# Kernel optimization log

Hardware: AMD Instinct MI355X
Metric: run time of the kernel (lower is better)

Reference implementation:

```python
import jax, jax.numpy as jnp
import numpy as np

F_DIM = 256; L = 4; B = 1; H = 160; W = 160; FH = 1024; N = B * H * W

def _ln(x, w, b):
    mu = jnp.mean(x, -1, keepdims=True)
    var = jnp.mean(jnp.square(x - mu), -1, keepdims=True)
    return (x - mu) * jax.lax.rsqrt(var + 1e-5) * w + b

def _conv(x, w, b, groups=1, pad=0):
    y = jax.lax.conv_general_dilated(x, w, (1, 1), [(pad, pad), (pad, pad)],
                                     dimension_numbers=('NCHW', 'OIHW', 'NCHW'),
                                     feature_group_count=groups)
    return y + b[None, :, None, None]

def _wsilu(x):
    return jax.nn.sigmoid(4.0 * x) * x

def setup_inputs() -> dict:
    key = jax.random.key(0)
    ks = iter(jax.random.split(key, 40))
    nk = lambda: next(ks)
    s = 1.0 / np.sqrt(F_DIM).astype(np.float32)
    inp = {}
    inp['x'] = jax.random.normal(nk(), (B, 1, H, W), jnp.float32)
    inp['cin_w1'] = jax.random.normal(nk(), (F_DIM, 1, 1, 1), jnp.float32)
    inp['cin_b1'] = jnp.zeros((F_DIM,), jnp.float32)
    inp['cin_w2'] = jax.random.normal(nk(), (F_DIM, 1, 7, 7), jnp.float32) * 0.15
    inp['cin_b2'] = jnp.zeros((F_DIM,), jnp.float32)
    inp['ln0_w'] = jnp.ones((F_DIM,), jnp.float32); inp['ln0_b'] = jnp.zeros((F_DIM,), jnp.float32)
    inp['ln1_w'] = jnp.ones((L, F_DIM), jnp.float32); inp['ln1_b'] = jnp.zeros((L, F_DIM), jnp.float32)
    inp['ln2_w'] = jnp.ones((L, F_DIM), jnp.float32); inp['ln2_b'] = jnp.zeros((L, F_DIM), jnp.float32)
    for n in ['att_tmk', 'att_tmv', 'att_tmr', 'ffn_tmk', 'ffn_tmr']:
        inp[n] = jax.random.uniform(nk(), (L, F_DIM), jnp.float32)
    inp['att_tf'] = jax.random.normal(nk(), (L, F_DIM), jnp.float32) * 0.5
    # time_decay is stored as -exp(raw) by the module's loader
    inp['att_td'] = -jnp.exp(jax.random.normal(nk(), (L, F_DIM), jnp.float32) * 0.5)
    for n in ['att_kw', 'att_vw', 'att_rw', 'att_ow', 'ffn_rw']:
        inp[n] = jax.random.normal(nk(), (L, F_DIM, F_DIM), jnp.float32) * s
    inp['ffn_kw'] = jax.random.normal(nk(), (L, FH, F_DIM), jnp.float32) * s
    inp['ffn_vw'] = jax.random.normal(nk(), (L, F_DIM, FH), jnp.float32) * (1.0 / np.sqrt(FH).astype(np.float32))
    inp['spa_dw_w'] = jax.random.normal(nk(), (L, F_DIM, 1, 7, 7), jnp.float32) * 0.15
    inp['spa_dw_b'] = jnp.zeros((L, F_DIM), jnp.float32)
    inp['spa_pw_w'] = jax.random.normal(nk(), (L, F_DIM, F_DIM, 1, 1), jnp.float32) * s
    inp['spa_pw_b'] = jnp.zeros((L, F_DIM), jnp.float32)
    st = jnp.zeros((5 * L, N, F_DIM), jnp.float32)
    st = st.at[4::5].add(-1e30)  # pp slots start at -1e30 as in torch init
    inp['state0'] = st
    return inp

def reference(x, cin_w1, cin_b1, cin_w2, cin_b2, ln0_w, ln0_b, ln1_w, ln1_b,
              ln2_w, ln2_b, att_tmk, att_tmv, att_tmr, att_tf, att_td,
              att_kw, att_vw, att_rw, att_ow, ffn_tmk, ffn_tmr, ffn_kw,
              ffn_vw, ffn_rw, spa_dw_w, spa_dw_b, spa_pw_w, spa_pw_b, state0):
    # conv stem: 1x1 -> depthwise 7x7 -> WSiLU
    d = _conv(x, cin_w1, cin_b1)
    d = _wsilu(_conv(d, cin_w2, cin_b2, groups=F_DIM, pad=3))
    d = d.transpose(0, 2, 3, 1).reshape(N, F_DIM)  # 'b f h w -> (b h w) f'
    for i in range(L):
        if i == 0:
            d = _ln(d, ln0_w, ln0_b)
        # --- SA: single-step RWKV WKV ---
        xs = _ln(d, ln1_w[i], ln1_b[i])
        sp = state0[5 * i + 1]
        aa = state0[5 * i + 2]; bb = state0[5 * i + 3]; pp = state0[5 * i + 4]
        xk = xs * att_tmk[i] + sp * (1 - att_tmk[i])
        xv = xs * att_tmv[i] + sp * (1 - att_tmv[i])
        xr = xs * att_tmr[i] + sp * (1 - att_tmr[i])
        r = jax.nn.sigmoid(xr @ att_rw[i].T)
        k = xk @ att_kw[i].T
        v = xv @ att_vw[i].T
        ww = att_tf[i] + k
        p = jnp.maximum(pp, ww)
        e1 = jnp.exp(pp - p); e2 = jnp.exp(ww - p)
        wkv = (e1 * aa + e2 * v) / (e1 * bb + e2)
        d = d + (r * wkv) @ att_ow[i].T
        # --- FF: squared-relu channel mix ---
        xs = _ln(d, ln2_w[i], ln2_b[i])
        sp = state0[5 * i + 0]
        xk = xs * ffn_tmk[i] + sp * (1 - ffn_tmk[i])
        xr = xs * ffn_tmr[i] + sp * (1 - ffn_tmr[i])
        rr = jax.nn.sigmoid(xr @ ffn_rw[i].T)
        kk = jnp.square(jax.nn.relu(xk @ ffn_kw[i].T))
        d = d + rr * (kk @ ffn_vw[i].T)
        # --- spatial residual block ---
        img = d.reshape(B, H, W, F_DIM).transpose(0, 3, 1, 2)
        img = img + _conv(_conv(img, spa_dw_w[i], spa_dw_b[i], groups=F_DIM, pad=3),
                          spa_pw_w[i], spa_pw_b[i])
        d = img.transpose(0, 2, 3, 1).reshape(N, F_DIM)
    return d.reshape(B, H, W, F_DIM).transpose(0, 3, 1, 2)
```

## Files before the change

kernel.cpp:

```cpp
#include <hip/hip_runtime.h>
#include <hip/hip_bf16.h>
#include <cstdint>
#include <cstddef>

#define F_DIMC 256
#define FHC    1024
#define IMGH   160
#define IMGW   160
#define NTOK   25600
#define NLAY   4

using bf16 = __hip_bfloat16;
typedef __attribute__((ext_vector_type(8))) short bf16x8;
typedef __attribute__((ext_vector_type(4))) float f32x4;

#define MFMA16(a, b, c) __builtin_amdgcn_mfma_f32_16x16x32_bf16((a), (b), (c), 0, 0, 0)

struct Cvt6 { const float* s[6]; bf16* d[6]; };
__global__ void cvt6_k(Cvt6 a, int n) {
    int z = blockIdx.y;
    int i = blockIdx.x * 256 + threadIdx.x;
    if (i < n) a.d[z][i] = __float2bfloat16(a.s[z][i]);
}
struct Cvt2 { const float* s[2]; bf16* d[2]; };
__global__ void cvt2_k(Cvt2 a, int n) {
    int z = blockIdx.y;
    int i = blockIdx.x * 256 + threadIdx.x;
    if (i < n) a.d[z][i] = __float2bfloat16(a.s[z][i]);
}

__global__ void dw_transpose_k(const float* __restrict__ src, float* __restrict__ dst, int n) {
    int i = blockIdx.x * 256 + threadIdx.x;
    if (i < n) {
        int f = i & (F_DIMC - 1);
        int lt = i >> 8;
        int t = lt % 49;
        int l = lt / 49;
        dst[i] = src[((size_t)l * F_DIMC + f) * 49 + t];
    }
}

__global__ __launch_bounds__(256)
void stem2_k(const float* __restrict__ x, const float* __restrict__ w1,
             const float* __restrict__ b1, const float* __restrict__ w2,
             const float* __restrict__ b2, float* __restrict__ d)
{
    __shared__ float wts[49][64];
    __shared__ float w1s[64], b1s[64], b2s[64];
    __shared__ float2 xp[7][22];
    const int tid = threadIdx.x;
    const int f0 = blockIdx.y * 64;
    const int y = blockIdx.x / 10;
    const int x0 = (blockIdx.x % 10) * 16;

    for (int idx = tid; idx < 49 * 64; idx += 256) {
        int t = idx >> 6, fl = idx & 63;
        wts[t][fl] = w2[(f0 + fl) * 49 + t];
    }
    if (tid < 64) {
        w1s[tid] = w1[f0 + tid];
        b1s[tid] = b1[f0 + tid];
        b2s[tid] = b2[f0 + tid];
    }
    for (int p = tid; p < 7 * 22; p += 256) {
        int py = p / 22, px = p % 22;
        int gy = y + py - 3, gx = x0 + px - 3;
        bool ok = (unsigned)gy < IMGH && (unsigned)gx < IMGW;
        xp[py][px] = ok ? make_float2(x[gy * IMGW + gx], 1.f) : make_float2(0.f, 0.f);
    }
    __syncthreads();

    const int fl = tid & 63;
    const int xbase = (tid >> 6) * 4;
    float acc[4] = {0.f, 0.f, 0.f, 0.f}, accw[4] = {0.f, 0.f, 0.f, 0.f};
    #pragma unroll
    for (int ky = 0; ky < 7; ++ky) {
        float2 row[10];
        #pragma unroll
        for (int q = 0; q < 10; ++q) row[q] = xp[ky][xbase + q];
        #pragma unroll
        for (int kx = 0; kx < 7; ++kx) {
            float w = wts[ky * 7 + kx][fl];
            #pragma unroll
            for (int j = 0; j < 4; ++j) {
                acc[j]  = fmaf(row[j + kx].x, w, acc[j]);
                accw[j] = fmaf(row[j + kx].y, w, accw[j]);
            }
        }
    }
    const float w1f = w1s[fl], b1f = b1s[fl], b2f = b2s[fl];
    #pragma unroll
    for (int j = 0; j < 4; ++j) {
        float u = fmaf(w1f, acc[j], fmaf(b1f, accw[j], b2f));
        int pix = y * IMGW + x0 + xbase + j;
        d[(size_t)pix * F_DIMC + f0 + fl] = u / (1.f + __expf(-4.f * u));
    }
}

__device__ __forceinline__ void wave_ln(float* x, const float* __restrict__ w,
                                        const float* __restrict__ b, int lane)
{
    float s = x[0] + x[1] + x[2] + x[3];
    #pragma unroll
    for (int m = 1; m < 64; m <<= 1) s += __shfl_xor(s, m, 64);
    float mu = s * 0.00390625f;
    float t0 = x[0] - mu, t1 = x[1] - mu, t2 = x[2] - mu, t3 = x[3] - mu;
    float v = t0 * t0 + t1 * t1 + t2 * t2 + t3 * t3;
    #pragma unroll
    for (int m = 1; m < 64; m <<= 1) v += __shfl_xor(v, m, 64);
    float inv = rsqrtf(v * 0.00390625f + 1e-5f);
    f32x4 wv = *(const f32x4*)(w + lane * 4);
    f32x4 bv = *(const f32x4*)(b + lane * 4);
    x[0] = t0 * inv * wv[0] + bv[0];
    x[1] = t1 * inv * wv[1] + bv[1];
    x[2] = t2 * inv * wv[2] + bv[2];
    x[3] = t3 * inv * wv[3] + bv[3];
}

union Pack4 { bf16 h[4]; uint2 u; };

template<bool LN0>
__global__ __launch_bounds__(256)
void lnmix_sa_k(float* __restrict__ d, const float* __restrict__ sp,
                const float* __restrict__ ln0w, const float* __restrict__ ln0b,
                const float* __restrict__ lnw, const float* __restrict__ lnb,
                const float* __restrict__ tmk, const float* __restrict__ tmv,
                const float* __restrict__ tmr,
                bf16* __restrict__ xk, bf16* __restrict__ xv, bf16* __restrict__ xr)
{
    const int lane = threadIdx.x & 63;
    const int n = blockIdx.x * 4 + (threadIdx.x >> 6);
    const int base = n * F_DIMC + lane * 4;
    f32x4 dv = *(const f32x4*)(d + base);
    float xo[4] = {dv[0], dv[1], dv[2], dv[3]};
    if (LN0) {
        wave_ln(xo, ln0w, ln0b, lane);
        f32x4 o = {xo[0], xo[1], xo[2], xo[3]};
        *(f32x4*)(d + base) = o;
    }
    float xs[4] = {xo[0], xo[1], xo[2], xo[3]};
    wave_ln(xs, lnw, lnb, lane);
    f32x4 spv = *(const f32x4*)(sp + base);
    f32x4 k4 = *(const f32x4*)(tmk + lane * 4);
    f32x4 v4 = *(const f32x4*)(tmv + lane * 4);
    f32x4 r4 = *(const f32x4*)(tmr + lane * 4);
    Pack4 pk, pv, pr;
    #pragma unroll
    for (int j = 0; j < 4; ++j) {
        pk.h[j] = __float2bfloat16(xs[j] * k4[j] + spv[j] * (1.f - k4[j]));
        pv.h[j] = __float2bfloat16(xs[j] * v4[j] + spv[j] * (1.f - v4[j]));
        pr.h[j] = __float2bfloat16(xs[j] * r4[j] + spv[j] * (1.f - r4[j]));
    }
    *(uint2*)(xk + base) = pk.u;
    *(uint2*)(xv + base) = pv.u;
    *(uint2*)(xr + base) = pr.u;
}

__global__ __launch_bounds__(256)
void lnmix_ff_k(const float* __restrict__ d, const float* __restrict__ sp,
                const float* __restrict__ lnw, const float* __restrict__ lnb,
                const float* __restrict__ tmk, const float* __restrict__ tmr,
                bf16* __restrict__ xk, bf16* __restrict__ xr)
{
    const int lane = threadIdx.x & 63;
    const int n = blockIdx.x * 4 + (threadIdx.x >> 6);
    const int base = n * F_DIMC + lane * 4;
    f32x4 dv = *(const f32x4*)(d + base);
    float xs[4] = {dv[0], dv[1], dv[2], dv[3]};
    wave_ln(xs, lnw, lnb, lane);
    f32x4 spv = *(const f32x4*)(sp + base);
    f32x4 k4 = *(const f32x4*)(tmk + lane * 4);
    f32x4 r4 = *(const f32x4*)(tmr + lane * 4);
    Pack4 pk, pr;
    #pragma unroll
    for (int j = 0; j < 4; ++j) {
        pk.h[j] = __float2bfloat16(xs[j] * k4[j] + spv[j] * (1.f - k4[j]));
        pr.h[j] = __float2bfloat16(xs[j] * r4[j] + spv[j] * (1.f - r4[j]));
    }
    *(uint2*)(xk + base) = pk.u;
    *(uint2*)(xr + base) = pr.u;
}


__device__ __forceinline__ void stage_swz32(const bf16* __restrict__ g,
                                            bf16* lds, int tid)
{
    #pragma unroll
    for (int s = 0; s < 8; ++s) {
        int chunk = s * 256 + tid;
        int row = chunk >> 5, c16 = chunk & 31;
        int gc = c16 ^ (row & 15);
        __builtin_amdgcn_global_load_lds(
            (const __attribute__((address_space(1))) void*)(g + (size_t)row * 256 + gc * 8),
            (__attribute__((address_space(3))) void*)(lds + chunk * 8), 16, 0, 0);
    }
}

__device__ __forceinline__ void stage_swz16(const bf16* __restrict__ g, int lda,
                                            bf16* lds, int tid)
{
    #pragma unroll
    for (int s = 0; s < 8; ++s) {
        int chunk = s * 256 + tid;
        int row = chunk >> 4, c16 = chunk & 15;
        int gc = c16 ^ (row & 15);
        __builtin_amdgcn_global_load_lds(
            (const __attribute__((address_space(1))) void*)(g + (size_t)row * lda + gc * 8),
            (__attribute__((address_space(3))) void*)(lds + chunk * 8), 16, 0, 0);
    }
}

template<int RB>
__device__ __forceinline__ bf16x8 frag_ld(const bf16* lds, int row, int cb)
{
    return *(const bf16x8*)((const char*)lds + row * RB + (cb ^ ((row & 15) << 4)));
}

__device__ __forceinline__ void pass64(const bf16* __restrict__ Ag, const bf16* __restrict__ Bg,
                                       bf16* As, bf16* Bs, int tid, int wr, int wc,
                                       int lr, int hi, f32x4 (&acc)[2][2])
{
    stage_swz32(Ag, As, tid);
    stage_swz32(Bg, Bs, tid);
    __syncthreads();
    #pragma unroll
    for (int ks = 0; ks < 8; ++ks) {
        int cb = ks * 64 + hi * 16;
        bf16x8 a0 = frag_ld<512>(As, wr * 32 + lr, cb);
        bf16x8 a1 = frag_ld<512>(As, wr * 32 + 16 + lr, cb);
        bf16x8 b0 = frag_ld<512>(Bs, wc * 32 + lr, cb);
        bf16x8 b1 = frag_ld<512>(Bs, wc * 32 + 16 + lr, cb);
        acc[0][0] = MFMA16(a0, b0, acc[0][0]);
        acc[0][1] = MFMA16(a0, b1, acc[0][1]);
        acc[1][0] = MFMA16(a1, b0, acc[1][0]);
        acc[1][1] = MFMA16(a1, b1, acc[1][1]);
    }
    __syncthreads();
}

__global__ __launch_bounds__(256, 2)
void sawkv_k(const bf16* __restrict__ xk, const bf16* __restrict__ xv,
             const bf16* __restrict__ xr,
             const bf16* __restrict__ kw, const bf16* __restrict__ vw,
             const bf16* __restrict__ rw,
             const float* __restrict__ aa, const float* __restrict__ bb,
             const float* __restrict__ pp, const float* __restrict__ tf,
             bf16* __restrict__ ab)
{
    __shared__ __align__(16) bf16 As[64 * 256];
    __shared__ __align__(16) bf16 Bs[64 * 256];
    const int tid = threadIdx.x, lane = tid & 63, wave = tid >> 6;
    const int wr = wave >> 1, wc = wave & 1;
    const int lr = lane & 15, hi = lane >> 4;
    const int m0 = blockIdx.x * 64, n0 = blockIdx.y * 64;

    f32x4 ak[2][2], av[2][2], ar[2][2];
    #pragma unroll
    for (int m = 0; m < 2; ++m)
        #pragma unroll
        for (int n = 0; n < 2; ++n) {
            ak[m][n] = (f32x4){0.f, 0.f, 0.f, 0.f};
            av[m][n] = (f32x4){0.f, 0.f, 0.f, 0.f};
            ar[m][n] = (f32x4){0.f, 0.f, 0.f, 0.f};
        }

    pass64(xk + (size_t)m0 * 256, kw + (size_t)n0 * 256, As, Bs, tid, wr, wc, lr, hi, ak);
    pass64(xv + (size_t)m0 * 256, vw + (size_t)n0 * 256, As, Bs, tid, wr, wc, lr, hi, av);
    pass64(xr + (size_t)m0 * 256, rw + (size_t)n0 * 256, As, Bs, tid, wr, wc, lr, hi, ar);

    const int lr0 = hi * 4;
    #pragma unroll
    for (int mf = 0; mf < 2; ++mf)
        #pragma unroll
        for (int nf = 0; nf < 2; ++nf) {
            int col = n0 + wc * 32 + nf * 16 + lr;
            float tfc = tf[col];
            #pragma unroll
            for (int j = 0; j < 4; ++j) {
                int row = m0 + wr * 32 + mf * 16 + lr0 + j;
                size_t idx = (size_t)row * F_DIMC + col;
                float kk = ak[mf][nf][j], vv = av[mf][nf][j], rr = ar[mf][nf][j];
                float P = pp[idx];
                float ww = tfc + kk;
                float p = fmaxf(P, ww);
                float e1 = __expf(P - p), e2 = __expf(ww - p);
                float wkv = (e1 * aa[idx] + e2 * vv) / (e1 * bb[idx] + e2);
                ab[idx] = __float2bfloat16(wkv / (1.f + __expf(-rr)));
            }
        }
}

template<int EPI>
__global__ __launch_bounds__(256, 2)
void gemm128_k(const bf16* __restrict__ A, const bf16* __restrict__ Bw,
               int lda, int ldb, int K, int Nout,
               float* __restrict__ Cf, bf16* __restrict__ Cb,
               const float* __restrict__ bias)
{
    __shared__ __align__(16) bf16 As[128 * 128];
    __shared__ __align__(16) bf16 Bs[128 * 128];
    const int tid = threadIdx.x, lane = tid & 63, wave = tid >> 6;
    const int wr = wave >> 1, wc = wave & 1;
    const int lr = lane & 15, hi = lane >> 4;
    const int m0 = blockIdx.x * 128, n0 = blockIdx.y * 128;

    f32x4 acc[4][4];
    #pragma unroll
    for (int m = 0; m < 4; ++m)
        #pragma unroll
        for (int n = 0; n < 4; ++n) acc[m][n] = (f32x4){0.f, 0.f, 0.f, 0.f};

    for (int kt = 0; kt < K; kt += 128) {
        stage_swz16(A + (size_t)m0 * lda + kt, lda, As, tid);
        stage_swz16(Bw + (size_t)n0 * ldb + kt, ldb, Bs, tid);
        __syncthreads();
        #pragma unroll
        for (int ks = 0; ks < 4; ++ks) {
            int cb = ks * 64 + hi * 16;
            bf16x8 a[4], b[4];
            #pragma unroll
            for (int mf = 0; mf < 4; ++mf) a[mf] = frag_ld<256>(As, wr * 64 + mf * 16 + lr, cb);
            #pragma unroll
            for (int nf = 0; nf < 4; ++nf) b[nf] = frag_ld<256>(Bs, wc * 64 + nf * 16 + lr, cb);
            #pragma unroll
            for (int mf = 0; mf < 4; ++mf)
                #pragma unroll
                for (int nf = 0; nf < 4; ++nf)
                    acc[mf][nf] = MFMA16(a[mf], b[nf], acc[mf][nf]);
        }
        __syncthreads();
    }

    const int lr0 = hi * 4;
    #pragma unroll
    for (int mf = 0; mf < 4; ++mf)
        #pragma unroll
        for (int nf = 0; nf < 4; ++nf) {
            int col = n0 + wc * 64 + nf * 16 + lr;
            #pragma unroll
            for (int j = 0; j < 4; ++j) {
                int row = m0 + wr * 64 + mf * 16 + lr0 + j;
                size_t cidx = (size_t)row * Nout + col;
                float v = acc[mf][nf][j];
                if constexpr (EPI == 2) { float t = fmaxf(v, 0.f); Cb[cidx] = __float2bfloat16(t * t); }
                else if constexpr (EPI == 3) Cf[cidx] += v;
                else if constexpr (EPI == 5) Cf[cidx] += v + bias[col];
            }
        }
}

__global__ __launch_bounds__(256, 2)
void fvwrr_k(const bf16* __restrict__ kkb, const bf16* __restrict__ fvw,
             const bf16* __restrict__ xr, const bf16* __restrict__ rw,
             float* __restrict__ d)
{
    __shared__ __align__(16) bf16 As[128 * 128];
    __shared__ __align__(16) bf16 Bs[128 * 128];
    const int tid = threadIdx.x, lane = tid & 63, wave = tid >> 6;
    const int wr = wave >> 1, wc = wave & 1;
    const int lr = lane & 15, hi = lane >> 4;
    const int m0 = blockIdx.x * 128, n0 = blockIdx.y * 128;

    f32x4 arr[4][4], am[4][4];
    #pragma unroll
    for (int m = 0; m < 4; ++m)
        #pragma unroll
        for (int n = 0; n < 4; ++n) {
            arr[m][n] = (f32x4){0.f, 0.f, 0.f, 0.f};
            am[m][n]  = (f32x4){0.f, 0.f, 0.f, 0.f};
        }

    for (int kt = 0; kt < 256; kt += 128) {
        stage_swz16(xr + (size_t)m0 * 256 + kt, 256, As, tid);
        stage_swz16(rw + (size_t)n0 * 256 + kt, 256, Bs, tid);
        __syncthreads();
        #pragma unroll
        for (int ks = 0; ks < 4; ++ks) {
            int cb = ks * 64 + hi * 16;
            bf16x8 a[4], b[4];
            #pragma unroll
            for (int mf = 0; mf < 4; ++mf) a[mf] = frag_ld<256>(As, wr * 64 + mf * 16 + lr, cb);
            #pragma unroll
            for (int nf = 0; nf < 4; ++nf) b[nf] = frag_ld<256>(Bs, wc * 64 + nf * 16 + lr, cb);
            #pragma unroll
            for (int mf = 0; mf < 4; ++mf)
                #pragma unroll
                for (int nf = 0; nf < 4; ++nf)
                    arr[mf][nf] = MFMA16(a[mf], b[nf], arr[mf][nf]);
        }
        __syncthreads();
    }
    for (int kt = 0; kt < 1024; kt += 128) {
        stage_swz16(kkb + (size_t)m0 * 1024 + kt, 1024, As, tid);
        stage_swz16(fvw + (size_t)n0 * 1024 + kt, 1024, Bs, tid);
        __syncthreads();
        #pragma unroll
        for (int ks = 0; ks < 4; ++ks) {
            int cb = ks * 64 + hi * 16;
            bf16x8 a[4], b[4];
            #pragma unroll
            for (int mf = 0; mf < 4; ++mf) a[mf] = frag_ld<256>(As, wr * 64 + mf * 16 + lr, cb);
            #pragma unroll
            for (int nf = 0; nf < 4; ++nf) b[nf] = frag_ld<256>(Bs, wc * 64 + nf * 16 + lr, cb);
            #pragma unroll
            for (int mf = 0; mf < 4; ++mf)
                #pragma unroll
                for (int nf = 0; nf < 4; ++nf)
                    am[mf][nf] = MFMA16(a[mf], b[nf], am[mf][nf]);
        }
        __syncthreads();
    }

    const int lr0 = hi * 4;
    #pragma unroll
    for (int mf = 0; mf < 4; ++mf)
        #pragma unroll
        for (int nf = 0; nf < 4; ++nf) {
            int col = n0 + wc * 64 + nf * 16 + lr;
            #pragma unroll
            for (int j = 0; j < 4; ++j) {
                int row = m0 + wr * 64 + mf * 16 + lr0 + j;
                size_t cidx = (size_t)row * F_DIMC + col;
                float rr = 1.f / (1.f + __expf(-arr[mf][nf][j]));
                d[cidx] += rr * am[mf][nf][j];
            }
        }
}

__global__ __launch_bounds__(256)
void dwconv2_k(const float* __restrict__ d, const float* __restrict__ wT,
               const float* __restrict__ bias, bf16* __restrict__ out)
{
    __shared__ float patch[196][64];
    __shared__ float wt[49][64];
    const int lane = threadIdx.x;
    const int ty = threadIdx.y;
    const int f0 = blockIdx.z * 64;
    const int w0 = blockIdx.x * 8, h0 = blockIdx.y * 8;

    for (int t = ty; t < 49; t += 4) wt[t][lane] = wT[t * F_DIMC + f0 + lane];
    for (int p = ty; p < 196; p += 4) {
        int py = p / 14, px = p % 14;
        int gy = h0 + py - 3, gx = w0 + px - 3;
        float v = 0.f;
        if ((unsigned)gy < IMGH && (unsigned)gx < IMGW)
            v = d[(size_t)(gy * IMGW + gx) * F_DIMC + f0 + lane];
        patch[p][lane] = v;
    }
    __syncthreads();

    const float b = bias[f0 + lane];
    #pragma unroll
    for (int rr = 0; rr < 2; ++rr) {
        int ry = ty * 2 + rr;
        float acc8[8];
        #pragma unroll
        for (int px = 0; px < 8; ++px) acc8[px] = b;
        #pragma unroll
        for (int ky = 0; ky < 7; ++ky) {
            float rowv[14];
            #pragma unroll
            for (int c = 0; c < 14; ++c) rowv[c] = patch[(ry + ky) * 14 + c][lane];
            #pragma unroll
            for (int kx = 0; kx < 7; ++kx) {
                float w = wt[ky * 7 + kx][lane];
                #pragma unroll
                for (int px = 0; px < 8; ++px)
                    acc8[px] = fmaf(rowv[px + kx], w, acc8[px]);
            }
        }
        #pragma unroll
        for (int px = 0; px < 8; ++px)
            out[(size_t)((h0 + ry) * IMGW + (w0 + px)) * F_DIMC + f0 + lane] = __float2bfloat16(acc8[px]);
    }
}

__global__ __launch_bounds__(256)
void transpose_out_k(const float* __restrict__ d, float* __restrict__ out)
{
    __shared__ float tile[32][33];
    const int n0 = blockIdx.x * 32, f0 = blockIdx.y * 32;
    const int tx = threadIdx.x, ty = threadIdx.y;
    for (int r = ty; r < 32; r += 8) tile[r][tx] = d[(size_t)(n0 + r) * F_DIMC + f0 + tx];
    __syncthreads();
    for (int r = ty; r < 32; r += 8) out[(size_t)(f0 + r) * NTOK + n0 + tx] = tile[tx][r];
}

extern "C" void kernel_launch(void* const* d_in, const int* in_sizes, int n_in,
                              void* d_out, int out_size, void* d_ws, size_t ws_size,
                              hipStream_t stream)
{
    if (n_in < 30) return;
    const float* x        = (const float*)d_in[0];
    const float* cin_w1   = (const float*)d_in[1];
    const float* cin_b1   = (const float*)d_in[2];
    const float* cin_w2   = (const float*)d_in[3];
    const float* cin_b2   = (const float*)d_in[4];
    const float* ln0_w    = (const float*)d_in[5];
    const float* ln0_b    = (const float*)d_in[6];
    const float* ln1_w    = (const float*)d_in[7];
    const float* ln1_b    = (const float*)d_in[8];
    const float* ln2_w    = (const float*)d_in[9];
    const float* ln2_b    = (const float*)d_in[10];
    const float* att_tmk  = (const float*)d_in[11];
    const float* att_tmv  = (const float*)d_in[12];
    const float* att_tmr  = (const float*)d_in[13];
    const float* ffn_tmk  = (const float*)d_in[14];
    const float* ffn_tmr  = (const float*)d_in[15];
    const float* att_tf   = (const float*)d_in[16];
    const float* att_kw   = (const float*)d_in[18];
    const float* att_vw   = (const float*)d_in[19];
    const float* att_rw   = (const float*)d_in[20];
    const float* att_ow   = (const float*)d_in[21];
    const float* ffn_rw   = (const float*)d_in[22];
    const float* ffn_kw   = (const float*)d_in[23];
    const float* ffn_vw   = (const float*)d_in[24];
    const float* spa_dw_w = (const float*)d_in[25];
    const float* spa_dw_b = (const float*)d_in[26];
    const float* spa_pw_w = (const float*)d_in[27];
    const float* spa_pw_b = (const float*)d_in[28];
    const float* state0   = (const float*)d_in[29];
    float* out = (float*)d_out;

    const size_t NF = (size_t)NTOK * F_DIMC;
    char* wsp = (char*)d_ws;
    size_t off = 0;
    auto alloc = [&](size_t bytes) -> void* {
        void* p = wsp + off;
        off += (bytes + 255) & ~(size_t)255;
        return p;
    };
    float* d_buf = (float*)alloc(NF * 4);
    bf16*  xk    = (bf16*)alloc(NF * 2);
    bf16*  xv    = (bf16*)alloc(NF * 2);
    bf16*  xr    = (bf16*)alloc(NF * 2);
    bf16*  ab    = (bf16*)alloc(NF * 2);
    bf16*  kkb   = (bf16*)alloc((size_t)NTOK * FHC * 2);
    const size_t WSQ = (size_t)NLAY * F_DIMC * F_DIMC;
    bf16* kwb  = (bf16*)alloc(WSQ * 2);
    bf16* vwb  = (bf16*)alloc(WSQ * 2);
    bf16* rwb  = (bf16*)alloc(WSQ * 2);
    bf16* owb  = (bf16*)alloc(WSQ * 2);
    bf16* frwb = (bf16*)alloc(WSQ * 2);
    bf16* fkwb = (bf16*)alloc((size_t)NLAY * FHC * F_DIMC * 2);
    bf16* fvwb = (bf16*)alloc((size_t)NLAY * F_DIMC * FHC * 2);
    bf16* pwb  = (bf16*)alloc(WSQ * 2);
    float* dwT = (float*)alloc((size_t)NLAY * 49 * F_DIMC * 4);
    if (off > ws_size) return;

    {
        Cvt6 c6;
        c6.s[0] = att_kw;  c6.d[0] = kwb;
        c6.s[1] = att_vw;  c6.d[1] = vwb;
        c6.s[2] = att_rw;  c6.d[2] = rwb;
        c6.s[3] = att_ow;  c6.d[3] = owb;
        c6.s[4] = ffn_rw;  c6.d[4] = frwb;
        c6.s[5] = spa_pw_w; c6.d[5] = pwb;
        cvt6_k<<<dim3(((int)WSQ + 255) / 256, 6), dim3(256), 0, stream>>>(c6, (int)WSQ);
        Cvt2 c2;
        c2.s[0] = ffn_kw; c2.d[0] = fkwb;
        c2.s[1] = ffn_vw; c2.d[1] = fvwb;
        int n2 = NLAY * FHC * F_DIMC;
        cvt2_k<<<dim3((n2 + 255) / 256, 2), dim3(256), 0, stream>>>(c2, n2);
        int n = NLAY * 49 * F_DIMC;
        dw_transpose_k<<<dim3((n + 255) / 256), dim3(256), 0, stream>>>(spa_dw_w, dwT, n);
    }

    stem2_k<<<dim3(IMGH * 10, 4), dim3(256), 0, stream>>>(x, cin_w1, cin_b1, cin_w2, cin_b2, d_buf);

    for (int i = 0; i < NLAY; ++i) {
        const float* sp_ff = state0 + (size_t)(5 * i + 0) * NF;
        const float* sp_at = state0 + (size_t)(5 * i + 1) * NF;
        const float* aa    = state0 + (size_t)(5 * i + 2) * NF;
        const float* bb    = state0 + (size_t)(5 * i + 3) * NF;
        const float* pp    = state0 + (size_t)(5 * i + 4) * NF;
        const float* l1w = ln1_w + i * F_DIMC, *l1b = ln1_b + i * F_DIMC;
        const float* l2w = ln2_w + i * F_DIMC, *l2b = ln2_b + i * F_DIMC;
        const float* tmk = att_tmk + i * F_DIMC, *tmv = att_tmv + i * F_DIMC, *tmr = att_tmr + i * F_DIMC;
        const float* ftmk = ffn_tmk + i * F_DIMC, *ftmr = ffn_tmr + i * F_DIMC;
        const float* tf = att_tf + i * F_DIMC;
        const bf16* kw_i  = kwb  + (size_t)i * F_DIMC * F_DIMC;
        const bf16* vw_i  = vwb  + (size_t)i * F_DIMC * F_DIMC;
        const bf16* rw_i  = rwb  + (size_t)i * F_DIMC * F_DIMC;
        const bf16* ow_i  = owb  + (size_t)i * F_DIMC * F_DIMC;
        const bf16* frw_i = frwb + (size_t)i * F_DIMC * F_DIMC;
        const bf16* fkw_i = fkwb + (size_t)i * FHC * F_DIMC;
        const bf16* fvw_i = fvwb + (size_t)i * F_DIMC * FHC;
        const bf16* pw_i  = pwb  + (size_t)i * F_DIMC * F_DIMC;
        const float* dwT_i = dwT + (size_t)i * 49 * F_DIMC;
        const float* dwb_i = spa_dw_b + i * F_DIMC;
        const float* pwbias_i = spa_pw_b + i * F_DIMC;

        if (i == 0)
            lnmix_sa_k<true><<<dim3(NTOK / 4), dim3(256), 0, stream>>>(
                d_buf, sp_at, ln0_w, ln0_b, l1w, l1b, tmk, tmv, tmr, xk, xv, xr);
        else
            lnmix_sa_k<false><<<dim3(NTOK / 4), dim3(256), 0, stream>>>(
                d_buf, sp_at, ln0_w, ln0_b, l1w, l1b, tmk, tmv, tmr, xk, xv, xr);

        sawkv_k<<<dim3(NTOK / 64, 4), dim3(256), 0, stream>>>(
            xk, xv, xr, kw_i, vw_i, rw_i, aa, bb, pp, tf, ab);

        gemm128_k<3><<<dim3(NTOK / 128, 2), dim3(256), 0, stream>>>(
            ab, ow_i, F_DIMC, F_DIMC, F_DIMC, F_DIMC, d_buf, nullptr, nullptr);

        lnmix_ff_k<<<dim3(NTOK / 4), dim3(256), 0, stream>>>(d_buf, sp_ff, l2w, l2b, ftmk, ftmr, xk, xr);

        gemm128_k<2><<<dim3(NTOK / 128, 8), dim3(256), 0, stream>>>(
            xk, fkw_i, F_DIMC, F_DIMC, F_DIMC, FHC, nullptr, kkb, nullptr);

        fvwrr_k<<<dim3(NTOK / 128, 2), dim3(256), 0, stream>>>(kkb, fvw_i, xr, frw_i, d_buf);

        dwconv2_k<<<dim3(IMGW / 8, IMGH / 8, 4), dim3(64, 4), 0, stream>>>(d_buf, dwT_i, dwb_i, ab);

        gemm128_k<5><<<dim3(NTOK / 128, 2), dim3(256), 0, stream>>>(
            ab, pw_i, F_DIMC, F_DIMC, F_DIMC, F_DIMC, d_buf, nullptr, pwbias_i);
    }

    transpose_out_k<<<dim3(NTOK / 32, F_DIMC / 32), dim3(32, 8), 0, stream>>>(d_buf, out);
}
```

Baseline: 1.952 ms.

## Store residual in fp16 and split KV/R projection from WKV elementwise

Converts the residual stream buffer from fp32 to fp16 throughout all kernels that read or update it, halving its memory traffic. Replaces the fused 64x64 three-pass K/V/R GEMM plus WKV epilogue with a batched 128x128 GEMM writing fp16 K, V and sigmoid(R), followed by a separate elementwise WKV kernel. Makes the GEMM K dimension a compile-time template parameter with unrolled loops. The split adds extra intermediate round trips, and accumulating residual updates in fp16 risks precision loss.

After: 1.931 ms. About the same (-1.1%).

```diff
diff --git a/kernel.cpp b/kernel.cpp
--- a/kernel.cpp
+++ b/kernel.cpp
@@ -11,10 +11,14 @@
 #define NLAY   4
 
 using bf16 = __hip_bfloat16;
+using f16  = _Float16;
 typedef __attribute__((ext_vector_type(8))) short bf16x8;
 typedef __attribute__((ext_vector_type(4))) float f32x4;
 
 #define MFMA16(a, b, c) __builtin_amdgcn_mfma_f32_16x16x32_bf16((a), (b), (c), 0, 0, 0)
+
+union H4 { f16 h[4]; uint2 u; };
+union Pack4 { bf16 h[4]; uint2 u; };
 
 struct Cvt6 { const float* s[6]; bf16* d[6]; };
 __global__ void cvt6_k(Cvt6 a, int n) {
@@ -43,7 +47,7 @@
 __global__ __launch_bounds__(256)
 void stem2_k(const float* __restrict__ x, const float* __restrict__ w1,
              const float* __restrict__ b1, const float* __restrict__ w2,
-             const float* __restrict__ b2, float* __restrict__ d)
+             const float* __restrict__ b2, f16* __restrict__ d)
 {
     __shared__ float wts[49][64];
     __shared__ float w1s[64], b1s[64], b2s[64];
@@ -93,7 +97,7 @@
     for (int j = 0; j < 4; ++j) {
         float u = fmaf(w1f, acc[j], fmaf(b1f, accw[j], b2f));
         int pix = y * IMGW + x0 + xbase + j;
-        d[(size_t)pix * F_DIMC + f0 + fl] = u / (1.f + __expf(-4.f * u));
+        d[(size_t)pix * F_DIMC + f0 + fl] = (f16)(u / (1.f + __expf(-4.f * u)));
     }
 }
 
@@ -117,11 +121,9 @@
     x[3] = t3 * inv * wv[3] + bv[3];
 }
 
-union Pack4 { bf16 h[4]; uint2 u; };
-
 template<bool LN0>
 __global__ __launch_bounds__(256)
-void lnmix_sa_k(float* __restrict__ d, const float* __restrict__ sp,
+void lnmix_sa_k(f16* __restrict__ d, const float* __restrict__ sp,
                 const float* __restrict__ ln0w, const float* __restrict__ ln0b,
                 const float* __restrict__ lnw, const float* __restrict__ lnb,
                 const float* __restrict__ tmk, const float* __restrict__ tmv,
@@ -131,12 +133,14 @@
     const int lane = threadIdx.x & 63;
     const int n = blockIdx.x * 4 + (threadIdx.x >> 6);
     const int base = n * F_DIMC + lane * 4;
-    f32x4 dv = *(const f32x4*)(d + base);
-    float xo[4] = {dv[0], dv[1], dv[2], dv[3]};
+    H4 hv; hv.u = *(const uint2*)(d + base);
+    float xo[4] = {(float)hv.h[0], (float)hv.h[1], (float)hv.h[2], (float)hv.h[3]};
     if (LN0) {
         wave_ln(xo, ln0w, ln0b, lane);
-        f32x4 o = {xo[0], xo[1], xo[2], xo[3]};
-        *(f32x4*)(d + base) = o;
+        H4 o;
+        #pragma unroll
+        for (int j = 0; j < 4; ++j) o.h[j] = (f16)xo[j];
+        *(uint2*)(d + base) = o.u;
     }
     float xs[4] = {xo[0], xo[1], xo[2], xo[3]};
     wave_ln(xs, lnw, lnb, lane);
@@ -157,7 +161,7 @@
 }
 
 __global__ __launch_bounds__(256)
-void lnmix_ff_k(const float* __restrict__ d, const float* __restrict__ sp,
+void lnmix_ff_k(const f16* __restrict__ d, const float* __restrict__ sp,
                 const float* __restrict__ lnw, const float* __restrict__ lnb,
                 const float* __restrict__ tmk, const float* __restrict__ tmr,
                 bf16* __restrict__ xk, bf16* __restrict__ xr)
@@ -165,8 +169,8 @@
     const int lane = threadIdx.x & 63;
     const int n = blockIdx.x * 4 + (threadIdx.x >> 6);
     const int base = n * F_DIMC + lane * 4;
-    f32x4 dv = *(const f32x4*)(d + base);
-    float xs[4] = {dv[0], dv[1], dv[2], dv[3]};
+    H4 hv; hv.u = *(const uint2*)(d + base);
+    float xs[4] = {(float)hv.h[0], (float)hv.h[1], (float)hv.h[2], (float)hv.h[3]};
     wave_ln(xs, lnw, lnb, lane);
     f32x4 spv = *(const f32x4*)(sp + base);
     f32x4 k4 = *(const f32x4*)(tmk + lane * 4);
@@ -181,19 +185,32 @@
     *(uint2*)(xr + base) = pr.u;
 }
 
-
-__device__ __forceinline__ void stage_swz32(const bf16* __restrict__ g,
-                                            bf16* lds, int tid)
-{
-    #pragma unroll
-    for (int s = 0; s < 8; ++s) {
-        int chunk = s * 256 + tid;
-        int row = chunk >> 5, c16 = chunk & 31;
-        int gc = c16 ^ (row & 15);
-        __builtin_amdgcn_global_load_lds(
-            (const __attribute__((address_space(1))) void*)(g + (size_t)row * 256 + gc * 8),
-            (__attribute__((address_space(3))) void*)(lds + chunk * 8), 16, 0, 0);
-    }
+__global__ __launch_bounds__(256)
+void wkv_k(const f16* __restrict__ r_, const f16* __restrict__ k_,
+           const f16* __restrict__ v_, const float* __restrict__ aa,
+           const float* __restrict__ bb, const float* __restrict__ pp,
+           const float* __restrict__ tf, bf16* __restrict__ out)
+{
+    int i = blockIdx.x * 256 + threadIdx.x;
+    int f0 = (i << 2) & (F_DIMC - 1);
+    H4 r4; r4.u = *(const uint2*)(r_ + (size_t)i * 4);
+    H4 k4; k4.u = *(const uint2*)(k_ + (size_t)i * 4);
+    H4 v4; v4.u = *(const uint2*)(v_ + (size_t)i * 4);
+    f32x4 a4 = *(const f32x4*)(aa + (size_t)i * 4);
+    f32x4 b4 = *(const f32x4*)(bb + (size_t)i * 4);
+    f32x4 p4 = *(const f32x4*)(pp + (size_t)i * 4);
+    f32x4 t4 = *(const f32x4*)(tf + f0);
+    Pack4 po;
+    #pragma unroll
+    for (int j = 0; j < 4; ++j) {
+        float ww = t4[j] + (float)k4.h[j];
+        float p = fmaxf(p4[j], ww);
+        float e1 = __expf(p4[j] - p);
+        float e2 = __expf(ww - p);
+        float wkv = (e1 * a4[j] + e2 * (float)v4.h[j]) / (e1 * b4[j] + e2);
+        po.h[j] = __float2bfloat16((float)r4.h[j] * wkv);
+    }
+    *(uint2*)(out + (size_t)i * 4) = po.u;
 }
 
 __device__ __forceinline__ void stage_swz16(const bf16* __restrict__ g, int lda,
@@ -216,85 +233,69 @@
     return *(const bf16x8*)((const char*)lds + row * RB + (cb ^ ((row & 15) << 4)));
 }
 
-__device__ __forceinline__ void pass64(const bf16* __restrict__ Ag, const bf16* __restrict__ Bg,
-                                       bf16* As, bf16* Bs, int tid, int wr, int wc,
-                                       int lr, int hi, f32x4 (&acc)[2][2])
-{
-    stage_swz32(Ag, As, tid);
-    stage_swz32(Bg, Bs, tid);
-    __syncthreads();
-    #pragma unroll
-    for (int ks = 0; ks < 8; ++ks) {
-        int cb = ks * 64 + hi * 16;
-        bf16x8 a0 = frag_ld<512>(As, wr * 32 + lr, cb);
-        bf16x8 a1 = frag_ld<512>(As, wr * 32 + 16 + lr, cb);
-        bf16x8 b0 = frag_ld<512>(Bs, wc * 32 + lr, cb);
-        bf16x8 b1 = frag_ld<512>(Bs, wc * 32 + 16 + lr, cb);
-        acc[0][0] = MFMA16(a0, b0, acc[0][0]);
-        acc[0][1] = MFMA16(a0, b1, acc[0][1]);
-        acc[1][0] = MFMA16(a1, b0, acc[1][0]);
-        acc[1][1] = MFMA16(a1, b1, acc[1][1]);
-    }
-    __syncthreads();
-}
-
+struct G3 { const bf16* A[3]; const bf16* W[3]; f16* C[3]; };
 __global__ __launch_bounds__(256, 2)
-void sawkv_k(const bf16* __restrict__ xk, const bf16* __restrict__ xv,
-             const bf16* __restrict__ xr,
-             const bf16* __restrict__ kw, const bf16* __restrict__ vw,
-             const bf16* __restrict__ rw,
-             const float* __restrict__ aa, const float* __restrict__ bb,
-             const float* __restrict__ pp, const float* __restrict__ tf,
-             bf16* __restrict__ ab)
-{
-    __shared__ __align__(16) bf16 As[64 * 256];
-    __shared__ __align__(16) bf16 Bs[64 * 256];
+void gemm3_k(G3 g)
+{
+    __shared__ __align__(16) bf16 As[128 * 128];
+    __shared__ __align__(16) bf16 Bs[128 * 128];
+    const int z = blockIdx.z;
+    const bf16* __restrict__ A  = g.A[z];
+    const bf16* __restrict__ Bw = g.W[z];
+    f16* __restrict__ C         = g.C[z];
     const int tid = threadIdx.x, lane = tid & 63, wave = tid >> 6;
     const int wr = wave >> 1, wc = wave & 1;
     const int lr = lane & 15, hi = lane >> 4;
-    const int m0 = blockIdx.x * 64, n0 = blockIdx.y * 64;
-
-    f32x4 ak[2][2], av[2][2], ar[2][2];
-    #pragma unroll
-    for (int m = 0; m < 2; ++m)
-        #pragma unroll
-        for (int n = 0; n < 2; ++n) {
-            ak[m][n] = (f32x4){0.f, 0.f, 0.f, 0.f};
-            av[m][n] = (f32x4){0.f, 0.f, 0.f, 0.f};
-            ar[m][n] = (f32x4){0.f, 0.f, 0.f, 0.f};
-        }
-
-    pass64(xk + (size_t)m0 * 256, kw + (size_t)n0 * 256, As, Bs, tid, wr, wc, lr, hi, ak);
-    pass64(xv + (size_t)m0 * 256, vw + (size_t)n0 * 256, As, Bs, tid, wr, wc, lr, hi, av);
-    pass64(xr + (size_t)m0 * 256, rw + (size_t)n0 * 256, As, Bs, tid, wr, wc, lr, hi, ar);
+    const int m0 = blockIdx.x * 128, n0 = blockIdx.y * 128;
+
+    f32x4 acc[4][4];
+    #pragma unroll
+    for (int m = 0; m < 4; ++m)
+        #pragma unroll
+        for (int n = 0; n < 4; ++n) acc[m][n] = (f32x4){0.f, 0.f, 0.f, 0.f};
+
+    #pragma unroll
+    for (int kt = 0; kt < 256; kt += 128) {
+        stage_swz16(A + (size_t)m0 * 256 + kt, 256, As, tid);
+        stage_swz16(Bw + (size_t)n0 * 256 + kt, 256, Bs, tid);
+        __syncthreads();
+        #pragma unroll
+        for (int ks = 0; ks < 4; ++ks) {
+            int cb = ks * 64 + hi * 16;
+            bf16x8 a[4], b[4];
+            #pragma unroll
+            for (int mf = 0; mf < 4; ++mf) a[mf] = frag_ld<256>(As, wr * 64 + mf * 16 + lr, cb);
+            #pragma unroll
+            for (int nf = 0; nf < 4; ++nf) b[nf] = frag_ld<256>(Bs, wc * 64 + nf * 16 + lr, cb);
+            #pragma unroll
+            for (int mf = 0; mf < 4; ++mf)
+                #pragma unroll
+                for (int nf = 0; nf < 4; ++nf)
+                    acc[mf][nf] = MFMA16(a[mf], b[nf], acc[mf][nf]);
+        }
+        __syncthreads();
+    }
 
     const int lr0 = hi * 4;
     #pragma unroll
-    for (int mf = 0; mf < 2; ++mf)
-        #pragma unroll
-        for (int nf = 0; nf < 2; ++nf) {
-            int col = n0 + wc * 32 + nf * 16 + lr;
-            float tfc = tf[col];
+    for (int mf = 0; mf < 4; ++mf)
+        #pragma unroll
+        for (int nf = 0; nf < 4; ++nf) {
+            int col = n0 + wc * 64 + nf * 16 + lr;
             #pragma unroll
             for (int j = 0; j < 4; ++j) {
-                int row = m0 + wr * 32 + mf * 16 + lr0 + j;
-                size_t idx = (size_t)row * F_DIMC + col;
-                float kk = ak[mf][nf][j], vv = av[mf][nf][j], rr = ar[mf][nf][j];
-                float P = pp[idx];
-                float ww = tfc + kk;
-                float p = fmaxf(P, ww);
-                float e1 = __expf(P - p), e2 = __expf(ww - p);
-                float wkv = (e1 * aa[idx] + e2 * vv) / (e1 * bb[idx] + e2);
-                ab[idx] = __float2bfloat16(wkv / (1.f + __expf(-rr)));
+                int row = m0 + wr * 64 + mf * 16 + lr0 + j;
+                float v = acc[mf][nf][j];
+                if (z == 2) v = 1.f / (1.f + __expf(-v));
+                C[(size_t)row * F_DIMC + col] = (f16)v;
             }
         }
 }
 
-template<int EPI>
+template<int EPI, int K>
 __global__ __launch_bounds__(256, 2)
 void gemm128_k(const bf16* __restrict__ A, const bf16* __restrict__ Bw,
-               int lda, int ldb, int K, int Nout,
-               float* __restrict__ Cf, bf16* __restrict__ Cb,
+               int Nout, f16* __restrict__ Cf, bf16* __restrict__ Cb,
                const float* __restrict__ bias)
 {
     __shared__ __align__(16) bf16 As[128 * 128];
@@ -310,9 +311,10 @@
         #pragma unroll
         for (int n = 0; n < 4; ++n) acc[m][n] = (f32x4){0.f, 0.f, 0.f, 0.f};
 
+    #pragma unroll
     for (int kt = 0; kt < K; kt += 128) {
-        stage_swz16(A + (size_t)m0 * lda + kt, lda, As, tid);
-        stage_swz16(Bw + (size_t)n0 * ldb + kt, ldb, Bs, tid);
+        stage_swz16(A + (size_t)m0 * K + kt, K, As, tid);
+        stage_swz16(Bw + (size_t)n0 * K + kt, K, Bs, tid);
         __syncthreads();
         #pragma unroll
         for (int ks = 0; ks < 4; ++ks) {
@@ -343,8 +345,8 @@
                 size_t cidx = (size_t)row * Nout + col;
                 float v = acc[mf][nf][j];
                 if constexpr (EPI == 2) { float t = fmaxf(v, 0.f); Cb[cidx] = __float2bfloat16(t * t); }
-                else if constexpr (EPI == 3) Cf[cidx] += v;
-                else if constexpr (EPI == 5) Cf[cidx] += v + bias[col];
+                else if constexpr (EPI == 3) Cf[cidx] = (f16)((float)Cf[cidx] + v);
+                else if constexpr (EPI == 5) Cf[cidx] = (f16)((float)Cf[cidx] + v + bias[col]);
             }
         }
 }
@@ -352,7 +354,7 @@
 __global__ __launch_bounds__(256, 2)
 void fvwrr_k(const bf16* __restrict__ kkb, const bf16* __restrict__ fvw,
              const bf16* __restrict__ xr, const bf16* __restrict__ rw,
-             float* __restrict__ d)
+             f16* __restrict__ d)
 {
     __shared__ __align__(16) bf16 As[128 * 128];
     __shared__ __align__(16) bf16 Bs[128 * 128];
@@ -370,6 +372,7 @@
             am[m][n]  = (f32x4){0.f, 0.f, 0.f, 0.f};
         }
 
+    #pragma unroll
     for (int kt = 0; kt < 256; kt += 128) {
         stage_swz16(xr + (size_t)m0 * 256 + kt, 256, As, tid);
         stage_swz16(rw + (size_t)n0 * 256 + kt, 256, Bs, tid);
@@ -390,6 +393,7 @@
         }
         __syncthreads();
     }
+    #pragma unroll
     for (int kt = 0; kt < 1024; kt += 128) {
         stage_swz16(kkb + (size_t)m0 * 1024 + kt, 1024, As, tid);
         stage_swz16(fvw + (size_t)n0 * 1024 + kt, 1024, Bs, tid);
@@ -422,13 +426,13 @@
                 int row = m0 + wr * 64 + mf * 16 + lr0 + j;
                 size_t cidx = (size_t)row * F_DIMC + col;
                 float rr = 1.f / (1.f + __expf(-arr[mf][nf][j]));
-                d[cidx] += rr * am[mf][nf][j];
+                d[cidx] = (f16)((float)d[cidx] + rr * am[mf][nf][j]);
             }
         }
 }
 
 __global__ __launch_bounds__(256)
-void dwconv2_k(const float* __restrict__ d, const float* __restrict__ wT,
+void dwconv2_k(const f16* __restrict__ d, const float* __restrict__ wT,
                const float* __restrict__ bias, bf16* __restrict__ out)
 {
     __shared__ float patch[196][64];
@@ -444,7 +448,7 @@
         int gy = h0 + py - 3, gx = w0 + px - 3;
         float v = 0.f;
         if ((unsigned)gy < IMGH && (unsigned)gx < IMGW)
-            v = d[(size_t)(gy * IMGW + gx) * F_DIMC + f0 + lane];
+            v = (float)d[(size_t)(gy * IMGW + gx) * F_DIMC + f0 + lane];
         patch[p][lane] = v;
     }
     __syncthreads();
@@ -476,12 +480,12 @@
 }
 
 __global__ __launch_bounds__(256)
-void transpose_out_k(const float* __restrict__ d, float* __restrict__ out)
+void transpose_out_k(const f16* __restrict__ d, float* __restrict__ out)
 {
     __shared__ float tile[32][33];
     const int n0 = blockIdx.x * 32, f0 = blockIdx.y * 32;
     const int tx = threadIdx.x, ty = threadIdx.y;
-    for (int r = ty; r < 32; r += 8) tile[r][tx] = d[(size_t)(n0 + r) * F_DIMC + f0 + tx];
+    for (int r = ty; r < 32; r += 8) tile[r][tx] = (float)d[(size_t)(n0 + r) * F_DIMC + f0 + tx];
     __syncthreads();
     for (int r = ty; r < 32; r += 8) out[(size_t)(f0 + r) * NTOK + n0 + tx] = tile[tx][r];
 }
@@ -530,7 +534,10 @@
         off += (bytes + 255) & ~(size_t)255;
         return p;
     };
-    float* d_buf = (float*)alloc(NF * 4);
+    f16*   d_buf = (f16*)alloc(NF * 2);
+    f16*   Gk    = (f16*)alloc(NF * 2);
+    f16*   Gv    = (f16*)alloc(NF * 2);
+    f16*   Gr    = (f16*)alloc(NF * 2);
     bf16*  xk    = (bf16*)alloc(NF * 2);
     bf16*  xv    = (bf16*)alloc(NF * 2);
     bf16*  xr    = (bf16*)alloc(NF * 2);
@@ -598,23 +605,28 @@
             lnmix_sa_k<false><<<dim3(NTOK / 4), dim3(256), 0, stream>>>(
                 d_buf, sp_at, ln0_w, ln0_b, l1w, l1b, tmk, tmv, tmr, xk, xv, xr);
 
-        sawkv_k<<<dim3(NTOK / 64, 4), dim3(256), 0, stream>>>(
-            xk, xv, xr, kw_i, vw_i, rw_i, aa, bb, pp, tf, ab);
-
-        gemm128_k<3><<<dim3(NTOK / 128, 2), dim3(256), 0, stream>>>(
-            ab, ow_i, F_DIMC, F_DIMC, F_DIMC, F_DIMC, d_buf, nullptr, nullptr);
+        G3 g3;
+        g3.A[0] = xk; g3.A[1] = xv; g3.A[2] = xr;
+        g3.W[0] = kw_i; g3.W[1] = vw_i; g3.W[2] = rw_i;
+        g3.C[0] = Gk; g3.C[1] = Gv; g3.C[2] = Gr;
+        gemm3_k<<<dim3(NTOK / 128, 2, 3), dim3(256), 0, stream>>>(g3);
+
+        wkv_k<<<dim3((int)(NF / 4 / 256)), dim3(256), 0, stream>>>(Gr, Gk, Gv, aa, bb, pp, tf, ab);
+
+        gemm128_k<3, 256><<<dim3(NTOK / 128, 2), dim3(256), 0, stream>>>(
+            ab, ow_i, F_DIMC, d_buf, nullptr, nullptr);
 
         lnmix_ff_k<<<dim3(NTOK / 4), dim3(256), 0, stream>>>(d_buf, sp_ff, l2w, l2b, ftmk, ftmr, xk, xr);
 
-        gemm128_k<2><<<dim3(NTOK / 128, 8), dim3(256), 0, stream>>>(
-            xk, fkw_i, F_DIMC, F_DIMC, F_DIMC, FHC, nullptr, kkb, nullptr);
+        gemm128_k<2, 256><<<dim3(NTOK / 128, 8), dim3(256), 0, stream>>>(
+            xk, fkw_i, FHC, nullptr, kkb, nullptr);
 
         fvwrr_k<<<dim3(NTOK / 128, 2), dim3(256), 0, stream>>>(kkb, fvw_i, xr, frw_i, d_buf);
 
         dwconv2_k<<<dim3(IMGW / 8, IMGH / 8, 4), dim3(64, 4), 0, stream>>>(d_buf, dwT_i, dwb_i, ab);
 
-        gemm128_k<5><<<dim3(NTOK / 128, 2), dim3(256), 0, stream>>>(
-            ab, pw_i, F_DIMC, F_DIMC, F_DIMC, F_DIMC, d_buf, nullptr, pwbias_i);
+        gemm128_k<5, 256><<<dim3(NTOK / 128, 2), dim3(256), 0, stream>>>(
+            ab, pw_i, F_DIMC, d_buf, nullptr, pwbias_i);
     }
 
     transpose_out_k<<<dim3(NTOK / 32, F_DIMC / 32), dim3(32, 8), 0, stream>>>(d_buf, out);
```
